# Kernel optimization log

Measured on AMD Instinct MI355X. Metric: run time of the kernel, lower is better.

Reference implementation:

```python
import jax, jax.numpy as jnp
import numpy as np

LRELU_SLOPE = 0.2
EPS = 1e-6

def _conv1x1(x, w):
    # x: [B,C,N,K], w: [O,C] -> [B,O,N,K]
    return jnp.einsum('bcnk,oc->bonk', x, w)

def _affine(x, g, b):
    # eval-mode BatchNorm with running mean=0, var=1 -> pure affine
    return x * g[None, :, None, None] + b[None, :, None, None]

def _lrelu(x):
    return jnp.where(x >= 0, x, LRELU_SLOPE * x)

def _head(x, w1, g, b, w2, b2):
    # Conv2d(2C,8,1,no bias) -> BN -> LeakyReLU -> (Dropout=id) -> Conv2d(8,1,1,bias)
    h = _lrelu(_affine(_conv1x1(x, w1), g, b))
    return _conv1x1(h, w2) + b2[None, :, None, None]  # [B,1,N,K]

def setup_inputs() -> dict:
    key = jax.random.key(0)
    ks = jax.random.split(key, 16)
    B, C2, N, K, O, H = 8, 128, 4096, 32, 64, 8
    inp = {
        'x': jax.random.normal(ks[0], (B, C2, N, K), jnp.float32),
        'w_trans': jax.random.normal(ks[1], (O, C2), jnp.float32) * 0.05,
        'g_trans': jax.random.uniform(ks[2], (O,), jnp.float32) + 0.5,
        'b_trans': jax.random.normal(ks[3], (O,), jnp.float32) * 0.1,
        'w_gate1': jax.random.normal(ks[4], (H, C2), jnp.float32) * 0.05,
        'g_gate': jax.random.uniform(ks[5], (H,), jnp.float32) + 0.5,
        'b_gate': jax.random.normal(ks[6], (H,), jnp.float32) * 0.1,
        'w_gate2': jax.random.normal(ks[7], (1, H), jnp.float32) * 0.3,
        'b_gate2': jax.random.normal(ks[8], (1,), jnp.float32) * 0.1,
        'w_attn1': jax.random.normal(ks[9], (H, C2), jnp.float32) * 0.05,
        'g_attn': jax.random.uniform(ks[10], (H,), jnp.float32) + 0.5,
        'b_attn': jax.random.normal(ks[11], (H,), jnp.float32) * 0.1,
        'w_attn2': jax.random.normal(ks[12], (1, H), jnp.float32) * 0.3,
        'b_attn2': jax.random.normal(ks[13], (1,), jnp.float32) * 0.1,
        'agg_alpha': jnp.zeros((), jnp.float32),
    }
    return inp

def reference(x, w_trans, g_trans, b_trans, w_gate1, g_gate, b_gate, w_gate2, b_gate2,
              w_attn1, g_attn, b_attn, w_attn2, b_attn2, agg_alpha):
    # mode='full', eval mode, tau=1.0, hard=False
    trans_feat = _lrelu(_affine(_conv1x1(x, w_trans), g_trans, b_trans))  # [B,O,N,K]
    gate_logits = _head(x, w_gate1, g_gate, b_gate, w_gate2, b_gate2)     # [B,1,N,K]
    # eval-mode gumbel_sigmoid_sample -> deterministic binary mask
    mask = (gate_logits >= 0).astype(x.dtype)                             # [B,1,N,K]
    attn_logits = _head(x, w_attn1, g_attn, b_attn, w_attn2, b_attn2)     # [B,1,N,K]
    attn_logits = attn_logits - jnp.max(attn_logits, axis=-1, keepdims=True)
    weights = jax.nn.softmax(attn_logits, axis=-1)
    # soft (hard=False) path: mask then renormalize
    weights = weights * mask
    weights = weights / (jnp.sum(weights, axis=-1, keepdims=True) + EPS)
    out_sum = jnp.sum(trans_feat * weights, axis=-1)   # [B,O,N]
    out_max = jnp.max(trans_feat, axis=-1)             # [B,O,N] (no masking when hard=False)
    alpha = jax.nn.sigmoid(agg_alpha)
    out = alpha * out_sum + (1.0 - alpha) * out_max
    return out, gate_logits
```

## Files before the change

kernel.cpp:

```cpp
#include <hip/hip_runtime.h>
#include <hip/hip_bf16.h>
#include <math.h>

#define NPB 131072
#define LRELU_SLOPE 0.2f
#define EPSV 1e-6f

typedef __attribute__((ext_vector_type(8))) short short8;
typedef __attribute__((ext_vector_type(4))) float f32x4;

static __device__ __forceinline__ unsigned short f2bf_rne(float f) {
    unsigned int u = __float_as_uint(f);
    u += 0x7fffu + ((u >> 16) & 1u);
    return (unsigned short)(u >> 16);
}

static __device__ __forceinline__ unsigned int cvt_pk_bf16(float f0, float f1) {
    __hip_bfloat162 h = __float22bfloat162_rn(make_float2(f0, f1));
    unsigned int r;
    __builtin_memcpy(&r, &h, 4);
    return r;
}

__global__ __launch_bounds__(256) void wt_kernel(
    const float* __restrict__ w_trans,
    const float* __restrict__ w_gate1,
    const float* __restrict__ w_attn1,
    unsigned short* __restrict__ Whi,
    unsigned short* __restrict__ Wlo)
{
    int i = blockIdx.x * 256 + threadIdx.x;
    if (i >= 80 * 128) return;
    int o = i >> 7;
    int c = i & 127;
    float v;
    if (o < 64)      v = w_trans[o * 128 + c];
    else if (o < 72) v = w_gate1[(o - 64) * 128 + c];
    else             v = w_attn1[(o - 72) * 128 + c];
    unsigned int u = __float_as_uint(v);
    Whi[i] = (unsigned short)(u >> 16);
    float hif = __uint_as_float(u & 0xffff0000u);
    Wlo[i] = f2bf_rne(v - hif);
}

__global__ __launch_bounds__(256, 4) void gsl_kernel(
    const float* __restrict__ x,
    const unsigned short* __restrict__ Whi,
    const unsigned short* __restrict__ Wlo,
    const float* __restrict__ g_trans, const float* __restrict__ b_trans,
    const float* __restrict__ g_gate,  const float* __restrict__ b_gate,
    const float* __restrict__ w_gate2, const float* __restrict__ b_gate2,
    const float* __restrict__ g_attn,  const float* __restrict__ b_attn,
    const float* __restrict__ w_attn2, const float* __restrict__ b_attn2,
    const float* __restrict__ agg_alpha,
    float* __restrict__ out0,
    float* __restrict__ outg)
{
    const int tid  = threadIdx.x;
    const int wid  = tid >> 6;
    const int lane = tid & 63;
    const int g    = lane >> 4;
    const int col  = lane & 15;

    const size_t p0 = (size_t)blockIdx.x * 128 + (size_t)wid * 32;
    const int b   = (int)(p0 >> 17);
    const int pin = (int)(p0 & (NPB - 1));
    const int n   = pin >> 5;

    const float* xq = x + (size_t)b * 128 * NPB + pin + col;

    f32x4 acc[5][2];
#pragma unroll
    for (int ot = 0; ot < 5; ++ot) {
        acc[ot][0] = (f32x4){0.f, 0.f, 0.f, 0.f};
        acc[ot][1] = (f32x4){0.f, 0.f, 0.f, 0.f};
    }

#pragma unroll
    for (int kk = 0; kk < 4; ++kk) {
        const int cbase = kk * 32 + 8 * g;

        float xv[16];
#pragma unroll
        for (int j = 0; j < 8; ++j) xv[j]     = xq[(size_t)(cbase + j) * NPB];
#pragma unroll
        for (int j = 0; j < 8; ++j) xv[8 + j] = xq[(size_t)(cbase + j) * NPB + 16];

        union U { unsigned int u[4]; short8 s; };
        U bh0, bl0, bh1, bl1;
#pragma unroll
        for (int jj = 0; jj < 4; ++jj) {
            float a0 = xv[2 * jj], a1 = xv[2 * jj + 1];
            unsigned int ua0 = __float_as_uint(a0), ua1 = __float_as_uint(a1);
            bh0.u[jj] = __builtin_amdgcn_perm(ua1, ua0, 0x07060302u);
            bl0.u[jj] = cvt_pk_bf16(a0 - __uint_as_float(ua0 & 0xffff0000u),
                                    a1 - __uint_as_float(ua1 & 0xffff0000u));

            float c0v = xv[8 + 2 * jj], c1v = xv[8 + 2 * jj + 1];
            unsigned int uc0 = __float_as_uint(c0v), uc1 = __float_as_uint(c1v);
            bh1.u[jj] = __builtin_amdgcn_perm(uc1, uc0, 0x07060302u);
            bl1.u[jj] = cvt_pk_bf16(c0v - __uint_as_float(uc0 & 0xffff0000u),
                                    c1v - __uint_as_float(uc1 & 0xffff0000u));
        }

#pragma unroll
        for (int ot = 0; ot < 5; ++ot) {
            const int wof = (ot * 16 + col) * 128 + cbase;
            short8 ahi = *(const short8*)(Whi + wof);
            short8 alo = *(const short8*)(Wlo + wof);
            acc[ot][0] = __builtin_amdgcn_mfma_f32_16x16x32_bf16(ahi, bh0.s, acc[ot][0], 0, 0, 0);
            acc[ot][1] = __builtin_amdgcn_mfma_f32_16x16x32_bf16(ahi, bh1.s, acc[ot][1], 0, 0, 0);
            acc[ot][0] = __builtin_amdgcn_mfma_f32_16x16x32_bf16(alo, bh0.s, acc[ot][0], 0, 0, 0);
            acc[ot][1] = __builtin_amdgcn_mfma_f32_16x16x32_bf16(alo, bh1.s, acc[ot][1], 0, 0, 0);
            acc[ot][0] = __builtin_amdgcn_mfma_f32_16x16x32_bf16(ahi, bl0.s, acc[ot][0], 0, 0, 0);
            acc[ot][1] = __builtin_amdgcn_mfma_f32_16x16x32_bf16(ahi, bl1.s, acc[ot][1], 0, 0, 0);
        }
    }

    const bool isGate = (g < 2);
    const int hbase = (g & 1) * 4;
    float hg[4], hb[4], hw[4];
#pragma unroll
    for (int r = 0; r < 4; ++r) {
        const int h = hbase + r;
        hg[r] = isGate ? g_gate[h]  : g_attn[h];
        hb[r] = isGate ? b_gate[h]  : b_attn[h];
        hw[r] = isGate ? w_gate2[h] : w_attn2[h];
    }
    float part0 = 0.f, part1 = 0.f;
#pragma unroll
    for (int r = 0; r < 4; ++r) {
        float v0 = fmaf(acc[4][0][r], hg[r], hb[r]);
        v0 = (v0 >= 0.f) ? v0 : LRELU_SLOPE * v0;
        part0 = fmaf(hw[r], v0, part0);
        float v1 = fmaf(acc[4][1][r], hg[r], hb[r]);
        v1 = (v1 >= 0.f) ? v1 : LRELU_SLOPE * v1;
        part1 = fmaf(hw[r], v1, part1);
    }
    float t0 = part0 + __shfl_xor(part0, 16);
    float t1 = part1 + __shfl_xor(part1, 16);
    float q0 = __shfl_xor(t0, 32);
    float q1 = __shfl_xor(t1, 32);
    const float bg2 = b_gate2[0], ba2 = b_attn2[0];
    float gl0 = (isGate ? t0 : q0) + bg2;
    float gl1 = (isGate ? t1 : q1) + bg2;
    float al0 = (isGate ? q0 : t0) + ba2;
    float al1 = (isGate ? q1 : t1) + ba2;

    if (lane < 16) {
        outg[p0 + col]      = gl0;
        outg[p0 + 16 + col] = gl1;
    }

    float m = fmaxf(al0, al1);
#pragma unroll
    for (int s = 1; s < 16; s <<= 1) m = fmaxf(m, __shfl_xor(m, s));
    float e0 = expf(al0 - m), e1 = expf(al1 - m);
    float w0m = (gl0 >= 0.f) ? e0 : 0.f;
    float w1m = (gl1 >= 0.f) ? e1 : 0.f;
    float s1 = e0 + e1;
    float sm = w0m + w1m;
#pragma unroll
    for (int s = 1; s < 16; s <<= 1) {
        s1 += __shfl_xor(s1, s);
        sm += __shfl_xor(sm, s);
    }
    const float inv = 1.f / (sm + EPSV * s1);
    const float wgt0 = w0m * inv;
    const float wgt1 = w1m * inv;

    const float aa = agg_alpha[0];
    const float alpha = 1.f / (1.f + expf(-aa));
    const float beta  = 1.f - alpha;

    float* outb = out0 + (size_t)b * 64 * 4096 + n;
#pragma unroll
    for (int ot = 0; ot < 4; ++ot) {
#pragma unroll
        for (int r = 0; r < 4; ++r) {
            const int o = ot * 16 + 4 * g + r;
            const float gt = g_trans[o], bt = b_trans[o];
            float v0 = fmaf(acc[ot][0][r], gt, bt);
            v0 = (v0 >= 0.f) ? v0 : LRELU_SLOPE * v0;
            float v1 = fmaf(acc[ot][1][r], gt, bt);
            v1 = (v1 >= 0.f) ? v1 : LRELU_SLOPE * v1;
            float sv = fmaf(v0, wgt0, v1 * wgt1);
            float mv = fmaxf(v0, v1);
#pragma unroll
            for (int s = 1; s < 16; s <<= 1) {
                sv += __shfl_xor(sv, s);
                mv = fmaxf(mv, __shfl_xor(mv, s));
            }
            if (col == 0)
                outb[(size_t)o * 4096] = fmaf(alpha, sv, beta * mv);
        }
    }
}

extern "C" void kernel_launch(void* const* d_in, const int* in_sizes, int n_in,
                              void* d_out, int out_size, void* d_ws, size_t ws_size,
                              hipStream_t stream) {
    const float* x        = (const float*)d_in[0];
    const float* w_trans  = (const float*)d_in[1];
    const float* g_trans  = (const float*)d_in[2];
    const float* b_trans  = (const float*)d_in[3];
    const float* w_gate1  = (const float*)d_in[4];
    const float* g_gate   = (const float*)d_in[5];
    const float* b_gate   = (const float*)d_in[6];
    const float* w_gate2  = (const float*)d_in[7];
    const float* b_gate2  = (const float*)d_in[8];
    const float* w_attn1  = (const float*)d_in[9];
    const float* g_attn   = (const float*)d_in[10];
    const float* b_attn   = (const float*)d_in[11];
    const float* w_attn2  = (const float*)d_in[12];
    const float* b_attn2  = (const float*)d_in[13];
    const float* agg_alpha= (const float*)d_in[14];

    float* out0 = (float*)d_out;
    float* outg = (float*)d_out + (size_t)8*64*4096;
    unsigned short* Whi = (unsigned short*)d_ws;
    unsigned short* Wlo = Whi + 80 * 128;

    wt_kernel<<<(80*128 + 255)/256, 256, 0, stream>>>(w_trans, w_gate1, w_attn1, Whi, Wlo);

    const int npix = 8 * NPB;
    gsl_kernel<<<npix / 128, 256, 0, stream>>>(
        x, Whi, Wlo, g_trans, b_trans, g_gate, b_gate, w_gate2, b_gate2,
        g_attn, b_attn, w_attn2, b_attn2, agg_alpha, out0, outg);
}
```

Before: 821.1 us.

## Stage x tiles through swizzled LDS with register double-buffered loads

Each block now covers 256 pixels with 512 threads. The x tile is loaded with coalesced 16-byte vector loads into registers, written to a rotated (bank-swizzled) shared-memory buffer, and read back per lane for the MFMA fragments, replacing scattered per-element global loads. Loads for the next 32-channel chunk are issued before computing the current one so memory latency overlaps with compute. The cost is 128KB of LDS per block and extra barriers, which caps occupancy at one block per CU.

```diff
diff --git a/kernel.cpp b/kernel.cpp
--- a/kernel.cpp
+++ b/kernel.cpp
@@ -5,6 +5,8 @@
 #define NPB 131072
 #define LRELU_SLOPE 0.2f
 #define EPSV 1e-6f
+#define PT 256
+#define LROW 256
 
 typedef __attribute__((ext_vector_type(8))) short short8;
 typedef __attribute__((ext_vector_type(4))) float f32x4;
@@ -43,7 +45,7 @@
     Wlo[i] = f2bf_rne(v - hif);
 }
 
-__global__ __launch_bounds__(256, 4) void gsl_kernel(
+__global__ __launch_bounds__(512, 2) void gsl_kernel(
     const float* __restrict__ x,
     const unsigned short* __restrict__ Whi,
     const unsigned short* __restrict__ Wlo,
@@ -56,18 +58,37 @@
     float* __restrict__ out0,
     float* __restrict__ outg)
 {
+    __shared__ float xs[128 * LROW];
+
     const int tid  = threadIdx.x;
     const int wid  = tid >> 6;
     const int lane = tid & 63;
     const int g    = lane >> 4;
     const int col  = lane & 15;
 
-    const size_t p0 = (size_t)blockIdx.x * 128 + (size_t)wid * 32;
-    const int b   = (int)(p0 >> 17);
-    const int pin = (int)(p0 & (NPB - 1));
-    const int n   = pin >> 5;
-
-    const float* xq = x + (size_t)b * 128 * NPB + pin + col;
+    const size_t P0 = (size_t)blockIdx.x * PT;
+    const int b    = (int)(P0 >> 17);
+    const int pin0 = (int)(P0 & (NPB - 1));
+
+    const float* xblk = x + (size_t)b * 128 * NPB + pin0;
+
+    auto ISSUE = [&](int q, f32x4* st) {
+#pragma unroll
+        for (int r = 0; r < 4; ++r) {
+            const int c = q * 32 + wid * 4 + r;
+            st[r] = *(const f32x4*)(xblk + (size_t)c * NPB + 4 * lane);
+        }
+    };
+    auto WRITE = [&](int q, const f32x4* st) {
+#pragma unroll
+        for (int r = 0; r < 4; ++r) {
+            const int c   = q * 32 + wid * 4 + r;
+            const int rot = (c >> 3) & 3;
+            const int p   = 4 * lane;
+            const int pe  = (p & ~31) | ((p + 8 * rot) & 31);
+            *(f32x4*)(&xs[c * LROW + pe]) = st[r];
+        }
+    };
 
     f32x4 acc[5][2];
 #pragma unroll
@@ -76,15 +97,16 @@
         acc[ot][1] = (f32x4){0.f, 0.f, 0.f, 0.f};
     }
 
-#pragma unroll
-    for (int kk = 0; kk < 4; ++kk) {
+    auto COMPUTE = [&](int kk) {
         const int cbase = kk * 32 + 8 * g;
 
         float xv[16];
 #pragma unroll
-        for (int j = 0; j < 8; ++j) xv[j]     = xq[(size_t)(cbase + j) * NPB];
-#pragma unroll
-        for (int j = 0; j < 8; ++j) xv[8 + j] = xq[(size_t)(cbase + j) * NPB + 16];
+        for (int j = 0; j < 8; ++j) {
+            const int base = (cbase + j) * LROW + wid * 32;
+            xv[j]     = xs[base + ((col + 8 * g) & 31)];
+            xv[8 + j] = xs[base + ((col + 16 + 8 * g) & 31)];
+        }
 
         union U { unsigned int u[4]; short8 s; };
         U bh0, bl0, bh1, bl1;
@@ -115,7 +137,20 @@
             acc[ot][0] = __builtin_amdgcn_mfma_f32_16x16x32_bf16(ahi, bl0.s, acc[ot][0], 0, 0, 0);
             acc[ot][1] = __builtin_amdgcn_mfma_f32_16x16x32_bf16(ahi, bl1.s, acc[ot][1], 0, 0, 0);
         }
-    }
+    };
+
+    f32x4 stA[4], stB[4];
+    ISSUE(0, stA); ISSUE(1, stB);
+    WRITE(0, stA); __syncthreads();
+    ISSUE(2, stA);
+    COMPUTE(0);
+    WRITE(1, stB); __syncthreads();
+    ISSUE(3, stB);
+    COMPUTE(1);
+    WRITE(2, stA); __syncthreads();
+    COMPUTE(2);
+    WRITE(3, stB); __syncthreads();
+    COMPUTE(3);
 
     const bool isGate = (g < 2);
     const int hbase = (g & 1) * 4;
@@ -147,6 +182,7 @@
     float al0 = (isGate ? q0 : t0) + ba2;
     float al1 = (isGate ? q1 : t1) + ba2;
 
+    const size_t p0 = P0 + (size_t)wid * 32;
     if (lane < 16) {
         outg[p0 + col]      = gl0;
         outg[p0 + 16 + col] = gl1;
@@ -173,6 +209,8 @@
     const float alpha = 1.f / (1.f + expf(-aa));
     const float beta  = 1.f - alpha;
 
+    const int pin = pin0 + wid * 32;
+    const int n   = pin >> 5;
     float* outb = out0 + (size_t)b * 64 * 4096 + n;
 #pragma unroll
     for (int ot = 0; ot < 4; ++ot) {
@@ -224,7 +262,7 @@
     wt_kernel<<<(80*128 + 255)/256, 256, 0, stream>>>(w_trans, w_gate1, w_attn1, Whi, Wlo);
 
     const int npix = 8 * NPB;
-    gsl_kernel<<<npix / 128, 256, 0, stream>>>(
+    gsl_kernel<<<npix / PT, 512, 0, stream>>>(
         x, Whi, Wlo, g_trans, b_trans, g_gate, b_gate, w_gate2, b_gate2,
         g_attn, b_attn, w_attn2, b_attn2, agg_alpha, out0, outg);
 }
```

Result: slower. 883.9 us (+7.6%).
